# Optimization experiments

Measured on AMD Instinct MI355X. Metric: run time of the kernel, lower is better.

The kernel has to match this reference:

```python
import jax, jax.numpy as jnp
import numpy as np

B, N, D, K = 4, 384, 64, 2  # batch, n_nodes, feat_dim, n_hops


def setup_inputs() -> dict:
    key = jax.random.key(0)
    k1, k2, k3 = jax.random.split(key, 3)
    A = jax.random.uniform(k1, (B, N, N, K), dtype=jnp.float32)      # weighted adjacency, one slice per hop
    X = jax.random.normal(k2, (B, N, D, K + 1), dtype=jnp.float32)   # node features over K+1 time steps
    W = jax.random.normal(k3, (D, D), dtype=jnp.float32) / np.sqrt(D)  # ffinal linear readout
    return {"A": A, "X": X, "W": W}


def _fcom(A, Y):
    # fcom: per-edge message broadcast. A: (b,N,N), Y: (b,N,D) -> (b,N,N,D)
    return A[..., None] * Y[:, None, :, :]


def reference(A, X, W):
    Kh = A.shape[-1]
    Ap = jnp.transpose(A, (0, 3, 1, 2))  # (b, K, N, N)
    Xp = jnp.transpose(X, (0, 3, 1, 2))  # (b, K+1, N, D)
    # single layer, layer_time = 0; finput = identity
    Xc = Xp
    Ac = Ap
    b, n, d = Xc.shape[0], Xc.shape[2], Xc.shape[3]

    # recursive k-hop walk aggregation: Y[k][-t] = sum_j fcom(A_{k-1}, Y[k-1][-t-1])
    Y = {1: {-t: Xc[:, t] for t in range(1, Kh + 1)}}
    for k in range(2, Kh + 1):
        Y[k] = {}
        for t in range(1, Kh + 1 - (k - 1)):
            # fcom(A, Y).sum(dim=2) == contraction over neighbor axis j
            Y[k][-t] = jnp.einsum('bij,bjd->bid', Ac[:, k - 1], Y[k - 1][-t - 1])

    # assemble Z: (b, K+1, N, N, D)
    idx = jnp.arange(n)
    Z0 = jnp.zeros((b, n, n, d), Xc.dtype).at[:, idx, idx, :].set(Xc[:, 0])  # diag_embed of self features
    Zk = [Z0] + [_fcom(Ac[:, 0], Y[k][-1]) for k in range(1, Kh + 1)]
    Z = jnp.stack(Zk, axis=1)

    # GNNnode.forward: sum over neighbors j (axis 3), sum over hop k (axis 1), linear readout
    agg = Z.sum(axis=3).sum(axis=1)  # (b, N, D)
    return agg @ W
```

## Files before the change

kernel.cpp:

```cpp
#include <hip/hip_runtime.h>

#define BB 4
#define NN 384
#define DD 64
#define XND (BB*NN*DD)


__global__ __launch_bounds__(256) void g1_pack(const float* __restrict__ X,
                                               float* __restrict__ ws) {
    const int idx = blockIdx.x * 256 + threadIdx.x;
    ws[idx] = X[(size_t)idx * 3 + 2];
}

#define FMA4(c, a, x)                          \
    c.x = fmaf(a, x.x, c.x);                   \
    c.y = fmaf(a, x.y, c.y);                   \
    c.z = fmaf(a, x.z, c.z);                   \
    c.w = fmaf(a, x.w, c.w);

#define RED4(c)                                                         \
    c.x += __shfl_xor(c.x, 16); c.y += __shfl_xor(c.y, 16);             \
    c.z += __shfl_xor(c.z, 16); c.w += __shfl_xor(c.w, 16);             \
    c.x += __shfl_xor(c.x, 32); c.y += __shfl_xor(c.y, 32);             \
    c.z += __shfl_xor(c.z, 32); c.w += __shfl_xor(c.w, 32);

__global__ __launch_bounds__(256) void g2_u(const float* __restrict__ A,
                                            const float* __restrict__ X,
                                            float* __restrict__ ws) {
    __shared__ float part[4][4][DD];
    const float* X2c = ws;
    float* U = ws + XND;

    const int tid = threadIdx.x, lane = tid & 63, ks = tid >> 6;
    const int dg = lane & 15, jsub = lane >> 4;
    const int lbid = ((int)blockIdx.x & 7) * 48 + ((int)blockIdx.x >> 3);
    const int b = lbid / 96, j0 = (lbid % 96) * 4;

    const int lb = ks * 96 + jsub;
    const float* xp = X2c + ((size_t)b * NN + lb) * DD + dg * 4;
    const float* a0 = A + (((size_t)b * NN + j0 + 0) * NN + lb) * 2 + 1;
    const float* a1 = A + (((size_t)b * NN + j0 + 1) * NN + lb) * 2 + 1;
    const float* a2 = A + (((size_t)b * NN + j0 + 2) * NN + lb) * 2 + 1;
    const float* a3 = A + (((size_t)b * NN + j0 + 3) * NN + lb) * 2 + 1;

    float4 c0{0,0,0,0}, c1{0,0,0,0}, c2{0,0,0,0}, c3{0,0,0,0};
    #pragma unroll 8
    for (int s = 0; s < 24; ++s) {
        float4 x = *(const float4*)(xp + s * 4 * DD);
        float v0 = a0[s * 8], v1 = a1[s * 8], v2 = a2[s * 8], v3 = a3[s * 8];
        FMA4(c0, v0, x) FMA4(c1, v1, x) FMA4(c2, v2, x) FMA4(c3, v3, x)
    }
    RED4(c0) RED4(c1) RED4(c2) RED4(c3)
    if (jsub == 0) {
        *(float4*)&part[ks][0][dg * 4] = c0;
        *(float4*)&part[ks][1][dg * 4] = c1;
        *(float4*)&part[ks][2][dg * 4] = c2;
        *(float4*)&part[ks][3][dg * 4] = c3;
    }
    __syncthreads();

    const int w = ks;
    float t = X[(((size_t)b * NN + j0 + w) * DD + lane) * 3 + 1];
    t += part[0][w][lane] + part[1][w][lane] + part[2][w][lane] + part[3][w][lane];
    U[((size_t)b * NN + j0 + w) * DD + lane] = t;
}

__global__ __launch_bounds__(256) void g3_out(const float* __restrict__ A,
                                              const float* __restrict__ X,
                                              const float* __restrict__ W,
                                              const float* __restrict__ ws,
                                              float* __restrict__ out) {
    __shared__ float part[4][4][DD];
    __shared__ float Ts[4][DD];
    __shared__ float Wsm[DD * DD];
    const float* U = ws + XND;

    const int tid = threadIdx.x, lane = tid & 63, ks = tid >> 6;
    const int dg = lane & 15, jsub = lane >> 4;
    const int lbid = ((int)blockIdx.x & 7) * 48 + ((int)blockIdx.x >> 3);
    const int b = lbid / 96, i0 = (lbid % 96) * 4;

    #pragma unroll
    for (int it = 0; it < 4; ++it) {
        int i4 = it * 256 + tid;
        *(float4*)&Wsm[i4 * 4] = ((const float4*)W)[i4];
    }

    const int lb = ks * 96 + jsub;
    const float* xp = U + ((size_t)b * NN + lb) * DD + dg * 4;
    const float* a0 = A + (((size_t)b * NN + i0 + 0) * NN + lb) * 2;
    const float* a1 = A + (((size_t)b * NN + i0 + 1) * NN + lb) * 2;
    const float* a2 = A + (((size_t)b * NN + i0 + 2) * NN + lb) * 2;
    const float* a3 = A + (((size_t)b * NN + i0 + 3) * NN + lb) * 2;

    float4 c0{0,0,0,0}, c1{0,0,0,0}, c2{0,0,0,0}, c3{0,0,0,0};
    #pragma unroll 8
    for (int s = 0; s < 24; ++s) {
        float4 x = *(const float4*)(xp + s * 4 * DD);
        float v0 = a0[s * 8], v1 = a1[s * 8], v2 = a2[s * 8], v3 = a3[s * 8];
        FMA4(c0, v0, x) FMA4(c1, v1, x) FMA4(c2, v2, x) FMA4(c3, v3, x)
    }
    RED4(c0) RED4(c1) RED4(c2) RED4(c3)
    if (jsub == 0) {
        *(float4*)&part[ks][0][dg * 4] = c0;
        *(float4*)&part[ks][1][dg * 4] = c1;
        *(float4*)&part[ks][2][dg * 4] = c2;
        *(float4*)&part[ks][3][dg * 4] = c3;
    }
    __syncthreads();

    const int w = ks;
    float t = X[(((size_t)b * NN + i0 + w) * DD + lane) * 3 + 0];
    t += part[0][w][lane] + part[1][w][lane] + part[2][w][lane] + part[3][w][lane];
    Ts[w][lane] = t;
    __syncthreads();

    float o = 0.f;
    #pragma unroll 16
    for (int d = 0; d < DD; ++d)
        o = fmaf(Ts[w][d], Wsm[d * DD + lane], o);
    out[((size_t)b * NN + i0 + w) * DD + lane] = o;
}

extern "C" void kernel_launch(void* const* d_in, const int* in_sizes, int n_in,
                              void* d_out, int out_size, void* d_ws, size_t ws_size,
                              hipStream_t stream) {
    const float* A = (const float*)d_in[0];
    const float* X = (const float*)d_in[1];
    const float* W = (const float*)d_in[2];
    float* out = (float*)d_out;
    float* ws  = (float*)d_ws;

    g1_pack<<<dim3(XND / 256), dim3(256), 0, stream>>>(X, ws);
    g2_u  <<<dim3(BB * NN / 4), dim3(256), 0, stream>>>(A, X, ws);
    g3_out<<<dim3(BB * NN / 4), dim3(256), 0, stream>>>(A, X, W, ws, out);
}
```

Measured before the change: 72.59 us.

## Fuse three kernels into one cooperative kernel with grid syncs

Merges the pack, U-computation and output kernels into a single cooperative launch of 384 blocks, separated by grid-wide barriers. W is also loaded into shared memory during the first phase. The aim is to remove the overhead and gaps of two extra kernel launches. The cost is the grid-sync overhead and the cooperative launch path, which requires all 384 blocks to be co-resident.

```diff
diff --git a/kernel.cpp b/kernel.cpp
--- a/kernel.cpp
+++ b/kernel.cpp
@@ -1,16 +1,13 @@
 #include <hip/hip_runtime.h>
+#include <hip/hip_cooperative_groups.h>
+
+namespace cg = cooperative_groups;
 
 #define BB 4
 #define NN 384
 #define DD 64
 #define XND (BB*NN*DD)
 
-
-__global__ __launch_bounds__(256) void g1_pack(const float* __restrict__ X,
-                                               float* __restrict__ ws) {
-    const int idx = blockIdx.x * 256 + threadIdx.x;
-    ws[idx] = X[(size_t)idx * 3 + 2];
-}
 
 #define FMA4(c, a, x)                          \
     c.x = fmaf(a, x.x, c.x);                   \
@@ -24,102 +21,101 @@
     c.x += __shfl_xor(c.x, 32); c.y += __shfl_xor(c.y, 32);             \
     c.z += __shfl_xor(c.z, 32); c.w += __shfl_xor(c.w, 32);
 
-__global__ __launch_bounds__(256) void g2_u(const float* __restrict__ A,
-                                            const float* __restrict__ X,
-                                            float* __restrict__ ws) {
+__global__ __launch_bounds__(256) void gnn_all(const float* __restrict__ A,
+                                               const float* __restrict__ X,
+                                               const float* __restrict__ W,
+                                               float* __restrict__ ws,
+                                               float* __restrict__ out) {
     __shared__ float part[4][4][DD];
-    const float* X2c = ws;
-    float* U = ws + XND;
+    __shared__ float Ts[4][DD];
+    __shared__ float Wsm[DD * DD];
 
     const int tid = threadIdx.x, lane = tid & 63, ks = tid >> 6;
     const int dg = lane & 15, jsub = lane >> 4;
     const int lbid = ((int)blockIdx.x & 7) * 48 + ((int)blockIdx.x >> 3);
-    const int b = lbid / 96, j0 = (lbid % 96) * 4;
+    const int b = lbid / 96, r0 = (lbid % 96) * 4;
 
-    const int lb = ks * 96 + jsub;
-    const float* xp = X2c + ((size_t)b * NN + lb) * DD + dg * 4;
-    const float* a0 = A + (((size_t)b * NN + j0 + 0) * NN + lb) * 2 + 1;
-    const float* a1 = A + (((size_t)b * NN + j0 + 1) * NN + lb) * 2 + 1;
-    const float* a2 = A + (((size_t)b * NN + j0 + 2) * NN + lb) * 2 + 1;
-    const float* a3 = A + (((size_t)b * NN + j0 + 3) * NN + lb) * 2 + 1;
+    const float* X2c = ws;
+    float* U = ws + XND;
 
-    float4 c0{0,0,0,0}, c1{0,0,0,0}, c2{0,0,0,0}, c3{0,0,0,0};
-    #pragma unroll 8
-    for (int s = 0; s < 24; ++s) {
-        float4 x = *(const float4*)(xp + s * 4 * DD);
-        float v0 = a0[s * 8], v1 = a1[s * 8], v2 = a2[s * 8], v3 = a3[s * 8];
-        FMA4(c0, v0, x) FMA4(c1, v1, x) FMA4(c2, v2, x) FMA4(c3, v3, x)
+    {
+        const int gidx = (int)blockIdx.x * 256 + tid;
+        ws[gidx] = X[(size_t)gidx * 3 + 2];
+        #pragma unroll
+        for (int it = 0; it < 4; ++it) {
+            int i4 = it * 256 + tid;
+            *(float4*)&Wsm[i4 * 4] = ((const float4*)W)[i4];
+        }
     }
-    RED4(c0) RED4(c1) RED4(c2) RED4(c3)
-    if (jsub == 0) {
-        *(float4*)&part[ks][0][dg * 4] = c0;
-        *(float4*)&part[ks][1][dg * 4] = c1;
-        *(float4*)&part[ks][2][dg * 4] = c2;
-        *(float4*)&part[ks][3][dg * 4] = c3;
+    cg::this_grid().sync();
+
+    {
+        const int lb = ks * 96 + jsub;
+        const float* xp = X2c + ((size_t)b * NN + lb) * DD + dg * 4;
+        const float* a0 = A + (((size_t)b * NN + r0 + 0) * NN + lb) * 2 + 1;
+        const float* a1 = A + (((size_t)b * NN + r0 + 1) * NN + lb) * 2 + 1;
+        const float* a2 = A + (((size_t)b * NN + r0 + 2) * NN + lb) * 2 + 1;
+        const float* a3 = A + (((size_t)b * NN + r0 + 3) * NN + lb) * 2 + 1;
+
+        float4 c0{0,0,0,0}, c1{0,0,0,0}, c2{0,0,0,0}, c3{0,0,0,0};
+        #pragma unroll 8
+        for (int s = 0; s < 24; ++s) {
+            float4 x = *(const float4*)(xp + s * 4 * DD);
+            float v0 = a0[s * 8], v1 = a1[s * 8], v2 = a2[s * 8], v3 = a3[s * 8];
+            FMA4(c0, v0, x) FMA4(c1, v1, x) FMA4(c2, v2, x) FMA4(c3, v3, x)
+        }
+        RED4(c0) RED4(c1) RED4(c2) RED4(c3)
+        if (jsub == 0) {
+            *(float4*)&part[ks][0][dg * 4] = c0;
+            *(float4*)&part[ks][1][dg * 4] = c1;
+            *(float4*)&part[ks][2][dg * 4] = c2;
+            *(float4*)&part[ks][3][dg * 4] = c3;
+        }
+        __syncthreads();
+
+        const int w = ks;
+        float t = X[(((size_t)b * NN + r0 + w) * DD + lane) * 3 + 1];
+        t += part[0][w][lane] + part[1][w][lane] + part[2][w][lane] + part[3][w][lane];
+        U[((size_t)b * NN + r0 + w) * DD + lane] = t;
     }
-    __syncthreads();
+    cg::this_grid().sync();
 
-    const int w = ks;
-    float t = X[(((size_t)b * NN + j0 + w) * DD + lane) * 3 + 1];
-    t += part[0][w][lane] + part[1][w][lane] + part[2][w][lane] + part[3][w][lane];
-    U[((size_t)b * NN + j0 + w) * DD + lane] = t;
-}
+    {
+        const int lb = ks * 96 + jsub;
+        const float* xp = U + ((size_t)b * NN + lb) * DD + dg * 4;
+        const float* a0 = A + (((size_t)b * NN + r0 + 0) * NN + lb) * 2;
+        const float* a1 = A + (((size_t)b * NN + r0 + 1) * NN + lb) * 2;
+        const float* a2 = A + (((size_t)b * NN + r0 + 2) * NN + lb) * 2;
+        const float* a3 = A + (((size_t)b * NN + r0 + 3) * NN + lb) * 2;
 
-__global__ __launch_bounds__(256) void g3_out(const float* __restrict__ A,
-                                              const float* __restrict__ X,
-                                              const float* __restrict__ W,
-                                              const float* __restrict__ ws,
-                                              float* __restrict__ out) {
-    __shared__ float part[4][4][DD];
-    __shared__ float Ts[4][DD];
-    __shared__ float Wsm[DD * DD];
-    const float* U = ws + XND;
+        float4 c0{0,0,0,0}, c1{0,0,0,0}, c2{0,0,0,0}, c3{0,0,0,0};
+        #pragma unroll 8
+        for (int s = 0; s < 24; ++s) {
+            float4 x = *(const float4*)(xp + s * 4 * DD);
+            float v0 = a0[s * 8], v1 = a1[s * 8], v2 = a2[s * 8], v3 = a3[s * 8];
+            FMA4(c0, v0, x) FMA4(c1, v1, x) FMA4(c2, v2, x) FMA4(c3, v3, x)
+        }
+        RED4(c0) RED4(c1) RED4(c2) RED4(c3)
+        if (jsub == 0) {
+            *(float4*)&part[ks][0][dg * 4] = c0;
+            *(float4*)&part[ks][1][dg * 4] = c1;
+            *(float4*)&part[ks][2][dg * 4] = c2;
+            *(float4*)&part[ks][3][dg * 4] = c3;
+        }
+        __syncthreads();
 
-    const int tid = threadIdx.x, lane = tid & 63, ks = tid >> 6;
-    const int dg = lane & 15, jsub = lane >> 4;
-    const int lbid = ((int)blockIdx.x & 7) * 48 + ((int)blockIdx.x >> 3);
-    const int b = lbid / 96, i0 = (lbid % 96) * 4;
+        const int w = ks;
+        float t = X[(((size_t)b * NN + r0 + w) * DD + lane) * 3 + 0];
+        t += part[0][w][lane] + part[1][w][lane] + part[2][w][lane] + part[3][w][lane];
+        Ts[w][lane] = t;
+        __syncthreads();
 
-    #pragma unroll
-    for (int it = 0; it < 4; ++it) {
-        int i4 = it * 256 + tid;
-        *(float4*)&Wsm[i4 * 4] = ((const float4*)W)[i4];
+        float o = 0.f;
+        #pragma unroll 16
+        for (int d = 0; d < DD; ++d)
+            o = fmaf(Ts[w][d], Wsm[d * DD + lane], o);
+        out[((size_t)b * NN + r0 + w) * DD + lane] = o;
     }
-
-    const int lb = ks * 96 + jsub;
-    const float* xp = U + ((size_t)b * NN + lb) * DD + dg * 4;
-    const float* a0 = A + (((size_t)b * NN + i0 + 0) * NN + lb) * 2;
-    const float* a1 = A + (((size_t)b * NN + i0 + 1) * NN + lb) * 2;
-    const float* a2 = A + (((size_t)b * NN + i0 + 2) * NN + lb) * 2;
-    const float* a3 = A + (((size_t)b * NN + i0 + 3) * NN + lb) * 2;
-
-    float4 c0{0,0,0,0}, c1{0,0,0,0}, c2{0,0,0,0}, c3{0,0,0,0};
-    #pragma unroll 8
-    for (int s = 0; s < 24; ++s) {
-        float4 x = *(const float4*)(xp + s * 4 * DD);
-        float v0 = a0[s * 8], v1 = a1[s * 8], v2 = a2[s * 8], v3 = a3[s * 8];
-        FMA4(c0, v0, x) FMA4(c1, v1, x) FMA4(c2, v2, x) FMA4(c3, v3, x)
-    }
-    RED4(c0) RED4(c1) RED4(c2) RED4(c3)
-    if (jsub == 0) {
-        *(float4*)&part[ks][0][dg * 4] = c0;
-        *(float4*)&part[ks][1][dg * 4] = c1;
-        *(float4*)&part[ks][2][dg * 4] = c2;
-        *(float4*)&part[ks][3][dg * 4] = c3;
-    }
-    __syncthreads();
-
-    const int w = ks;
-    float t = X[(((size_t)b * NN + i0 + w) * DD + lane) * 3 + 0];
-    t += part[0][w][lane] + part[1][w][lane] + part[2][w][lane] + part[3][w][lane];
-    Ts[w][lane] = t;
-    __syncthreads();
-
-    float o = 0.f;
-    #pragma unroll 16
-    for (int d = 0; d < DD; ++d)
-        o = fmaf(Ts[w][d], Wsm[d * DD + lane], o);
-    out[((size_t)b * NN + i0 + w) * DD + lane] = o;
 }
 
 extern "C" void kernel_launch(void* const* d_in, const int* in_sizes, int n_in,
@@ -131,7 +127,8 @@
     float* out = (float*)d_out;
     float* ws  = (float*)d_ws;
 
-    g1_pack<<<dim3(XND / 256), dim3(256), 0, stream>>>(X, ws);
-    g2_u  <<<dim3(BB * NN / 4), dim3(256), 0, stream>>>(A, X, ws);
-    g3_out<<<dim3(BB * NN / 4), dim3(256), 0, stream>>>(A, X, W, ws, out);
+    void* args[] = {(void*)&A, (void*)&X, (void*)&W, (void*)&ws, (void*)&out};
+    hipLaunchCooperativeKernel((const void*)gnn_all,
+                               dim3(BB * NN / 4), dim3(256),
+                               args, 0, stream);
 }
```

New measurement: 156.2 us. +115.2%, slower.
